# Kernel tuning notes

Hardware: AMD Instinct MI355X
Metric: run time of the kernel (lower is better)

The kernel has to match this reference:

```python
import jax, jax.numpy as jnp
import numpy as np

NEG = 0.01  # leaky_relu negative slope used throughout AttentiveFP


def _seg_softmax(logits, seg, num):
    # softmax over entries grouped by segment id (PyG softmax w/ 1e-16 eps)
    m = jax.ops.segment_max(logits, seg, num_segments=num)
    m = jnp.where(jnp.isfinite(m), m, 0.0)
    e = jnp.exp(logits - m[seg])
    s = jax.ops.segment_sum(e, seg, num_segments=num)
    return e / (s[seg] + 1e-16)


def _gru(x, h, wi, wh, bi, bh):
    # torch.nn.GRUCell math
    gi = x @ wi.T + bi
    gh = h @ wh.T + bh
    ir, iz, inn = jnp.split(gi, 3, axis=-1)
    hr, hz, hn = jnp.split(gh, 3, axis=-1)
    r = jax.nn.sigmoid(ir + hr)
    z = jax.nn.sigmoid(iz + hz)
    n = jnp.tanh(inn + r * hn)
    return (1.0 - z) * n + z * h


def _forward(x, edge_attr, mol_feats, lin1_w, lin1_b, gate_lin1_w, gate_lin2_w, gate_att_l, gate_att_r, gate_bias, grus_wi, grus_wh, grus_bi, grus_bh, atom_w, atom_att_src, atom_att_dst, atom_bias, mol_w, mol_att_src, mol_att_dst, mol_bias, lin2_w, lin2_b, fcm0_w, fcm0_b, fcm1_w, fcm1_b, fcm2_w, fcm2_b, fc0_w, fc0_b, fc1_w, fc1_b, fc2_w, fc2_b, fc3_w, fc3_b, fc4_w, fc4_b, edge_index, batch):
    N = x.shape[0]
    G = mol_feats.shape[0]
    src, dst = edge_index[0], edge_index[1]
    lrelu = lambda v: jax.nn.leaky_relu(v, NEG)
    # AttentiveFP (eval mode: dropout off)
    xh = lrelu(x @ lin1_w.T + lin1_b)  # [N,H]
    # --- GATEConv: edge-conditioned attention, add aggregation ---
    m = lrelu(jnp.concatenate([xh[src], edge_attr], axis=-1) @ gate_lin1_w.T)  # [E,H]
    a = lrelu(m @ gate_att_l + (xh @ gate_att_r)[dst])
    a = _seg_softmax(a, dst, N)
    h = jax.ops.segment_sum((m @ gate_lin2_w.T) * a[:, None], dst, num_segments=N) + gate_bias
    xh = jax.nn.relu(_gru(jax.nn.elu(h), xh, grus_wi[0], grus_wh[0], grus_bi[0], grus_bh[0]))
    # --- GATConv layers (num_layers-1 = 2, heads=1, no self loops) ---
    for l in range(2):
        xl = xh @ atom_w[l].T
        a = lrelu((xl @ atom_att_src[l])[src] + (xl @ atom_att_dst[l])[dst])
        a = _seg_softmax(a, dst, N)
        h = jax.ops.segment_sum(xl[src] * a[:, None], dst, num_segments=N) + atom_bias[l]
        xh = jax.nn.relu(_gru(jax.nn.elu(h), xh, grus_wi[1 + l], grus_wh[1 + l], grus_bi[1 + l], grus_bh[1 + l]))
    # --- attentive graph readout (num_timesteps = 3) ---
    out = jax.nn.relu(jax.ops.segment_sum(xh, batch, num_segments=G))  # [G,H]
    xm = xh @ mol_w.T            # atom-side lin (x fixed across timesteps)
    a_src = xm @ mol_att_src
    for _ in range(3):
        a = lrelu(a_src + ((out @ mol_w.T) @ mol_att_dst)[batch])
        a = _seg_softmax(a, batch, G)
        h = jax.ops.segment_sum(xm * a[:, None], batch, num_segments=G) + mol_bias
        out = jax.nn.relu(_gru(jax.nn.elu(h), out, grus_wi[3], grus_wh[3], grus_bi[3], grus_bh[3]))
    hg = out @ lin2_w.T + lin2_b  # [G,256]
    # --- mol-feature MLP branch (SiLU) ---
    hm = jax.nn.silu(mol_feats @ fcm0_w.T + fcm0_b)
    hm = jax.nn.silu(hm @ fcm1_w.T + fcm1_b)
    hm = jax.nn.silu(hm @ fcm2_w.T + fcm2_b)
    # --- fusion MLP ---
    hg = jnp.concatenate([hg, hm], axis=1)  # [G,512]
    hg = jax.nn.silu(hg @ fc0_w.T + fc0_b)
    hg = jax.nn.silu(hg @ fc1_w.T + fc1_b)
    hg = jax.nn.silu(hg @ fc2_w.T + fc2_b)
    hg = jax.nn.silu(hg @ fc3_w.T + fc3_b)
    return hg @ fc4_w.T + fc4_b  # [G,1]


def setup_inputs() -> dict:
    key = jax.random.key(0)
    ks = iter(jax.random.split(key, 64))
    def W(*shape):
        return jax.random.normal(next(ks), shape, jnp.float32) / np.float32(np.sqrt(shape[-1]))
    def B(*shape):
        return 0.02 * jax.random.normal(next(ks), shape, jnp.float32)
    N, E, G = 131072, 262144, 8192
    Fn, Fe, Fm, H = 64, 16, 200, 256
    return dict(
        x=jax.random.normal(next(ks), (N, Fn), jnp.float32),
        edge_attr=jax.random.normal(next(ks), (E, Fe), jnp.float32),
        mol_feats=jax.random.normal(next(ks), (G, Fm), jnp.float32),
        lin1_w=W(H, Fn), lin1_b=B(H),
        gate_lin1_w=W(H, H + Fe), gate_lin2_w=W(H, H),
        gate_att_l=W(H), gate_att_r=W(H), gate_bias=B(H),
        grus_wi=W(4, 3 * H, H), grus_wh=W(4, 3 * H, H), grus_bi=B(4, 3 * H), grus_bh=B(4, 3 * H),
        atom_w=W(2, H, H), atom_att_src=W(2, H), atom_att_dst=W(2, H), atom_bias=B(2, H),
        mol_w=W(H, H), mol_att_src=W(H), mol_att_dst=W(H), mol_bias=B(H),
        lin2_w=W(H, H), lin2_b=B(H),
        fcm0_w=W(H, Fm), fcm0_b=B(H), fcm1_w=W(H, H), fcm1_b=B(H), fcm2_w=W(H, H), fcm2_b=B(H),
        fc0_w=W(512, 512), fc0_b=B(512), fc1_w=W(512, 512), fc1_b=B(512),
        fc2_w=W(512, 512), fc2_b=B(512), fc3_w=W(128, 512), fc3_b=B(128),
        fc4_w=W(1, 128), fc4_b=B(1),
        edge_index=jax.random.randint(next(ks), (2, E), 0, N),
        batch=jnp.sort(jax.random.randint(next(ks), (N,), 0, G)),
    )


def reference(x, edge_attr, mol_feats, lin1_w, lin1_b, gate_lin1_w, gate_lin2_w, gate_att_l, gate_att_r, gate_bias, grus_wi, grus_wh, grus_bi, grus_bh, atom_w, atom_att_src, atom_att_dst, atom_bias, mol_w, mol_att_src, mol_att_dst, mol_bias, lin2_w, lin2_b, fcm0_w, fcm0_b, fcm1_w, fcm1_b, fcm2_w, fcm2_b, fc0_w, fc0_b, fc1_w, fc1_b, fc2_w, fc2_b, fc3_w, fc3_b, fc4_w, fc4_b, edge_index, batch):
    return _forward(x, edge_attr, mol_feats, lin1_w, lin1_b, gate_lin1_w, gate_lin2_w, gate_att_l, gate_att_r, gate_bias, grus_wi, grus_wh, grus_bi, grus_bh, atom_w, atom_att_src, atom_att_dst, atom_bias, mol_w, mol_att_src, mol_att_dst, mol_bias, lin2_w, lin2_b, fcm0_w, fcm0_b, fcm1_w, fcm1_b, fcm2_w, fcm2_b, fc0_w, fc0_b, fc1_w, fc1_b, fc2_w, fc2_b, fc3_w, fc3_b, fc4_w, fc4_b, edge_index, batch)
```

## Files before the change

kernel.cpp:

```cpp
#include <hip/hip_runtime.h>
#include <hip/hip_bf16.h>
#include <math.h>


typedef unsigned short u16;
typedef u16 u16x8 __attribute__((ext_vector_type(8)));
typedef short s16x8 __attribute__((ext_vector_type(8)));
typedef float f32x4 __attribute__((ext_vector_type(4)));

__device__ __forceinline__ float u2f(u16 u) { return __uint_as_float(((unsigned)u) << 16); }
__device__ __forceinline__ u16 f2u(float f) {
    return __builtin_bit_cast(u16, __float2bfloat16(f));
}

#define NEGS 0.01f

typedef const __attribute__((address_space(1))) unsigned gas1_t;
typedef __attribute__((address_space(3))) unsigned las3_t;
__device__ __forceinline__ void gload16(const void* g, void* l) {
    __builtin_amdgcn_global_load_lds((gas1_t*)g, (las3_t*)l, 16, 0, 0);
}

__device__ __forceinline__ unsigned fkey(float f) {
    unsigned u = __float_as_uint(f);
    return (u & 0x80000000u) ? ~u : (u | 0x80000000u);
}
__device__ __forceinline__ float funkey(unsigned k) {
    return (k & 0x80000000u) ? __uint_as_float(k ^ 0x80000000u) : __uint_as_float(~k);
}
#define KEY_NEG_INF 0x007FFFFFu

static inline int cdiv(int a, int b) { return (a + b - 1) / b; }

__global__ void fill_f32(float* p, float v, size_t n) {
    size_t i = (size_t)blockIdx.x * 256 + threadIdx.x;
    if (i < n) p[i] = v;
}
__global__ void fill_u32(unsigned* p, unsigned v, int n) {
    int i = blockIdx.x * 256 + threadIdx.x;
    if (i < n) p[i] = v;
}
__global__ void fill_km(unsigned* key, float* sum, int n) {
    int i = blockIdx.x * 256 + threadIdx.x;
    if (i < n) { key[i] = KEY_NEG_INF; sum[i] = 0.f; }
}
__global__ void copy_f2b(const float* s, u16* d, size_t n) {
    size_t i = (size_t)blockIdx.x * 256 + threadIdx.x;
    if (i < n) d[i] = f2u(s[i]);
}
__global__ void matvecT_k(const float* W, const float* a, float* v, int K, int Jout) {
    int j = blockIdx.x * 256 + threadIdx.x;
    if (j >= Jout) return;
    float s = 0.f;
    for (int k = 0; k < K; k++) s += W[(size_t)k * Jout + j] * a[k];
    v[j] = s;
}
__global__ void edge_add_lrelu_max(float* elog, const float* r, const int* dsti,
                                   unsigned* key, int E) {
    int i = blockIdx.x * 256 + threadIdx.x;
    if (i < E) {
        int d = dsti[i];
        float v = elog[i] + r[d];
        v = v > 0.f ? v : NEGS * v;
        elog[i] = v;
        atomicMax(&key[d], fkey(v));
    }
}
__global__ void pair_logit_max(float* elog, const float* s, const float* dd,
                               const int* srci, const int* dsti, unsigned* key, int E) {
    int i = blockIdx.x * 256 + threadIdx.x;
    if (i < E) {
        int d = dsti[i];
        float v = s[srci[i]] + dd[d];
        v = v > 0.f ? v : NEGS * v;
        elog[i] = v;
        atomicMax(&key[d], fkey(v));
    }
}
__global__ void node_logit_max(float* nlog, const float* asrc, const float* wg,
                               const int* batch, unsigned* key, int N) {
    int i = blockIdx.x * 256 + threadIdx.x;
    if (i < N) {
        int b = batch[i];
        float v = asrc[i] + wg[b];
        v = v > 0.f ? v : NEGS * v;
        nlog[i] = v;
        atomicMax(&key[b], fkey(v));
    }
}
__global__ void seg_exp_k(const float* logit, const int* idx, const unsigned* key,
                          float* ex, float* sum, int n) {
    int i = blockIdx.x * 256 + threadIdx.x;
    if (i < n) {
        float e = expf(logit[i] - funkey(key[idx[i]]));
        ex[i] = e;
        atomicAdd(&sum[idx[i]], e);
    }
}
__global__ void rowdot2_b(const u16* X, const float* v1, const float* v2,
                          float* o1, float* o2, int M) {
    int r = blockIdx.x * 4 + (threadIdx.x >> 6);
    int lane = threadIdx.x & 63;
    if (r >= M) return;
    const u16* row = X + (size_t)r * 256 + lane * 4;
    float p1 = 0.f, p2 = 0.f;
#pragma unroll
    for (int q = 0; q < 4; q++) {
        float xv = u2f(row[q]);
        p1 += xv * v1[lane * 4 + q];
        if (v2) p2 += xv * v2[lane * 4 + q];
    }
    for (int off = 32; off; off >>= 1) {
        p1 += __shfl_down(p1, off);
        if (v2) p2 += __shfl_down(p2, off);
    }
    if (lane == 0) {
        o1[r] = p1;
        if (v2) o2[r] = p2;
    }
}
__global__ void rowdot_f(const float* X, const float* v1, float* o1, int M) {
    int r = blockIdx.x * 4 + (threadIdx.x >> 6);
    int lane = threadIdx.x & 63;
    if (r >= M) return;
    float4 a = ((const float4*)(X + (size_t)r * 256))[lane];
    float4 b = ((const float4*)v1)[lane];
    float p1 = a.x * b.x + a.y * b.y + a.z * b.z + a.w * b.w;
    for (int off = 32; off; off >>= 1) p1 += __shfl_down(p1, off);
    if (lane == 0) o1[r] = p1;
}
__global__ void fc4_k(const float* X, const float* w, const float* b, float* out, int G) {
    int g = blockIdx.x * 4 + (threadIdx.x >> 6);
    int lane = threadIdx.x & 63;
    if (g >= G) return;
    float2 xv = ((const float2*)(X + (size_t)g * 128))[lane];
    float2 wv = ((const float2*)w)[lane];
    float p = xv.x * wv.x + xv.y * wv.y;
    for (int off = 32; off; off >>= 1) p += __shfl_down(p, off);
    if (lane == 0) out[g] = p + b[0];
}

__global__ void count_dst(const int* dst, int* cnt, int E) {
    int i = blockIdx.x * 256 + threadIdx.x;
    if (i < E) atomicAdd(&cnt[dst[i]], 1);
}
__global__ void scan1(const int* cnt, int* part, int N) {
    __shared__ int sm[256];
    int i = blockIdx.x * 256 + threadIdx.x;
    sm[threadIdx.x] = i < N ? cnt[i] : 0;
    __syncthreads();
    for (int off = 128; off; off >>= 1) {
        if (threadIdx.x < off) sm[threadIdx.x] += sm[threadIdx.x + off];
        __syncthreads();
    }
    if (threadIdx.x == 0) part[blockIdx.x] = sm[0];
}
__global__ void scan2(int* part, int nb) {
    __shared__ int a[1024], b[1024];
    int t = threadIdx.x;
    if (nb > 1024) {
        if (t == 0) {
            int acc = 0;
            for (int i = 0; i < nb; i++) { int v = part[i]; part[i] = acc; acc += v; }
        }
        return;
    }
    int v = t < nb ? part[t] : 0;
    a[t] = v;
    __syncthreads();
    int* cur = a; int* nxt = b;
    for (int off = 1; off < 1024; off <<= 1) {
        int s = cur[t] + (t >= off ? cur[t - off] : 0);
        nxt[t] = s;
        __syncthreads();
        int* tmp = cur; cur = nxt; nxt = tmp;
    }
    if (t < nb) part[t] = cur[t] - v;
}
__global__ void scan3(const int* cnt, const int* part, int* rowstart, int N) {
    __shared__ int a[256], b[256];
    int t = threadIdx.x;
    int i = blockIdx.x * 256 + t;
    int v = i < N ? cnt[i] : 0;
    a[t] = v;
    __syncthreads();
    int* cur = a; int* nxt = b;
    for (int off = 1; off < 256; off <<= 1) {
        int s = cur[t] + (t >= off ? cur[t - off] : 0);
        nxt[t] = s;
        __syncthreads();
        int* tmp = cur; cur = nxt; nxt = tmp;
    }
    if (i < N) rowstart[i] = part[blockIdx.x] + cur[t] - v;
}
__global__ void fill_csr(const int* dst, const int* rowstart, int* fillc,
                         int* eorder, int* erank, int E) {
    int e = blockIdx.x * 256 + threadIdx.x;
    if (e >= E) return;
    int d = dst[e];
    int s = rowstart[d] + atomicAdd(&fillc[d], 1);
    eorder[s] = e;
    erank[e] = s;
}
__global__ void chunk_dlo_k(const int* rowstart, const int* cnt, int N, int Crows,
                            int nch, int* dlo) {
    int c = blockIdx.x * 64 + threadIdx.x;
    if (c >= nch) return;
    int s0 = c * Crows;
    int lo = 0, hi = N;
    while (lo < hi) {
        int mid = (lo + hi) >> 1;
        if (rowstart[mid] + cnt[mid] > s0) hi = mid; else lo = mid + 1;
    }
    dlo[c] = lo;
}
template <int MODE>
__global__ void csr_red(const int* rowstart, const int* cnt, const int* eorder,
                        const float* ex, const float* sum, const int* srcE,
                        const u16* X, const u16* X2, int msplit,
                        int s0, int s1, const int* dlo,
                        u16* outH, u16* outL, int N) {
    int d;
    if (MODE == 1) {
        d = dlo[0] + blockIdx.x;
        if (d >= N) return;
        if (rowstart[d] >= s1) return;
    } else {
        d = blockIdx.x;
        if (d >= N) return;
    }
    int rs = rowstart[d], k = cnt[d];
    int lo = rs, hi = rs + k;
    if (MODE == 1) {
        if (lo < s0) lo = s0;
        if (hi > s1) hi = s1;
        if (lo >= hi) return;
    }
    float den = sum[d] + 1e-16f;
    int c = threadIdx.x;
    float acc = 0.f;
    for (int s = lo; s < hi; s++) {
        int e = eorder[s];
        float av = ex[e] / den;
        const u16* row;
        if (MODE == 0) row = X + (size_t)srcE[e] * 256;
        else if (MODE == 1) row = X + (size_t)(s - s0) * 256;
        else row = (e < msplit) ? X + (size_t)e * 256 : X2 + (size_t)(e - msplit) * 256;
        acc += av * u2f(row[c]);
    }
    size_t o = (size_t)d * 256 + c;
    if (MODE == 1) acc += u2f(outH[o]) + u2f(outL[o]);
    u16 hh = f2u(acc);
    outH[o] = hh;
    outL[o] = f2u(acc - u2f(hh));
}
__global__ void graph_bounds(const int* batch, int* gs, int* ge, int N) {
    int i = blockIdx.x * 256 + threadIdx.x;
    if (i >= N) return;
    int b = batch[i];
    atomicMin(&gs[b], i);
    atomicMax(&ge[b], i + 1);
}
template <bool RELU>
__global__ void seg_red(const int* gs, const int* ge, const u16* X, const float* sc,
                        const float* sum, float* out, int G) {
    int g = blockIdx.x;
    if (g >= G) return;
    int c = threadIdx.x;
    int s = gs[g], e = ge[g];
    float den = sc ? (sum[g] + 1e-16f) : 1.f;
    float acc = 0.f;
    if (s < e)
        for (int i = s; i < e; i++) {
            float v = u2f(X[(size_t)i * 256 + c]);
            if (sc) v *= sc[i] / den;
            acc += v;
        }
    out[(size_t)g * 256 + c] = RELU ? fmaxf(acc, 0.f) : acc;
}

__global__ void pack_w(const float* s1, const float* s2, int K1, int Ksrc,
                       int Nout, int Kp, u16* dst) {
    int idx = blockIdx.x * 256 + threadIdx.x;
    int kiters = Kp >> 5;
    int total = (Nout >> 7) * kiters * 512;
    if (idx >= total) return;
    int c = idx & 511;
    int rest = idx >> 9;
    int ki = rest % kiters, nb = rest / kiters;
    int n = (nb << 7) + (((c >> 6) & 7) << 4) + (c & 15);
    int k0 = (ki << 5) + (((c >> 4) & 3) << 3);
    u16x8 vh, vl;
#pragma unroll
    for (int j = 0; j < 8; j++) {
        int k = k0 + j;
        float f = 0.f;
        if (k < K1) f = s1[(size_t)n * K1 + k];
        else if (k < Ksrc) f = s2[(size_t)n * (Ksrc - K1) + (k - K1)];
        u16 h = f2u(f);
        vh[j] = h;
        vl[j] = f2u(f - u2f(h));
    }
    ((u16x8*)dst)[idx] = vh;
    ((u16x8*)dst)[idx + total] = vl;
}
__global__ void pack_gru_w(const float* wi, const float* wh, u16* dst) {
    int idx = blockIdx.x * 256 + threadIdx.x;
    const int total = 8 * 16 * 512;
    if (idx >= total) return;
    int c = idx & 511, rest = idx >> 9;
    int ki = rest & 15, nb = rest >> 4;
    int n = (nb << 7) + (((c >> 6) & 7) << 4) + (c & 15);
    int k0 = (ki << 5) + (((c >> 4) & 3) << 3);
    int grp = n >> 6, sub = (n >> 4) & 3, ch = grp * 16 + (n & 15);
    u16x8 vh, vl;
#pragma unroll
    for (int j = 0; j < 8; j++) {
        int k = k0 + j;
        float f;
        if (sub < 3) {
            int srow = sub * 256 + ch;
            f = (k < 256) ? wi[(size_t)srow * 256 + k]
                          : wh[(size_t)srow * 256 + (k - 256)];
        } else {
            f = (k < 256) ? 0.f : wh[(size_t)(512 + ch) * 256 + (k - 256)];
        }
        u16 h = f2u(f);
        vh[j] = h;
        vl[j] = f2u(f - u2f(h));
    }
    ((u16x8*)dst)[idx] = vh;
    ((u16x8*)dst)[idx + total] = vl;
}
__global__ void pack_gru_b(const float* bi, const float* bh, float* bp) {
    int n = blockIdx.x * 256 + threadIdx.x;
    if (n >= 1024) return;
    int grp = n >> 6, sub = (n >> 4) & 3, ch = grp * 16 + (n & 15);
    float v;
    if (sub == 0) v = bi[ch] + bh[ch];
    else if (sub == 1) v = bi[256 + ch] + bh[256 + ch];
    else if (sub == 2) v = bi[512 + ch] + bh[512 + ch];
    else v = bh[512 + ch];
    bp[n] = v;
}

struct p8 { u16x8 hi, lo; };
__device__ __forceinline__ u16x8 zero8() {
    u16x8 z;
#pragma unroll
    for (int j = 0; j < 8; j++) z[j] = 0;
    return z;
}
__device__ __forceinline__ p8 sp_zero() { p8 r; r.hi = zero8(); r.lo = zero8(); return r; }
__device__ __forceinline__ p8 sp_b(const u16* p) {
    p8 r;
    r.hi = *(const u16x8*)p;
    r.lo = zero8();
    return r;
}
__device__ __forceinline__ p8 sp_f(const float* p) {
    p8 r;
#pragma unroll
    for (int j = 0; j < 8; j++) {
        float x = p[j];
        u16 h = f2u(x);
        r.hi[j] = h;
        r.lo[j] = f2u(x - u2f(h));
    }
    return r;
}
__device__ __forceinline__ p8 sp_eluf(const float* p) {
    p8 r;
#pragma unroll
    for (int j = 0; j < 8; j++) {
        float x = p[j];
        float e = x > 0.f ? x : expm1f(x);
        u16 h = f2u(e);
        r.hi[j] = h;
        r.lo[j] = f2u(e - u2f(h));
    }
    return r;
}
template <int ALD>
__device__ __forceinline__ p8 ldA(bool valid, int k, int Ksrc, const u16* ab,
                                  const float* af, const float* x2) {
    if (!valid) return sp_zero();
    if (ALD == 1) {
        if (k >= Ksrc) return sp_zero();
        return sp_f(af + k);
    }
    if (ALD == 2 || ALD == 7) {
        if (k < 256) return sp_b(ab + k);
        if (k < 272) return sp_f(x2 + (k - 256));
        return sp_zero();
    }
    if (k < 256) return sp_eluf(af + k);
    return sp_f(x2 + (k - 256));
}
template <int ALD>
__device__ __forceinline__ bool lo_zero(int ki) {
    if (ALD == 2 || ALD == 7) return ki < 8;
    return false;
}
template <int ACT>
__device__ __forceinline__ float actf(float v) {
    if (ACT == 1) return v > 0.f ? v : NEGS * v;
    if (ACT == 3) return v / (1.f + expf(-v));
    return v;
}

template <int ALD, int ACT, int EPI>
__global__ __launch_bounds__(256, 4) void mgemm(
    int M, int Kp, int Ksrc,
    const float* Af, int lda, const u16* Ab, const u16* Ab2,
    const int* gidx, const float* X2f, const u16* Wp, const float* b1,
    float* Cf, u16* Cb, u16* Cb2, int csplit, int ldc,
    const float* attv, float* dotout, const int* didx) {
    __shared__ u16x8 lsAll[2048];
    u16x8* lsAh = lsAll;
    u16x8* lsAl = lsAll + 512;
    u16x8* lsWh = lsAll + 1024;
    u16x8* lsWl = lsAll + 1536;
    const int t = threadIdx.x;
    const int m0 = blockIdx.x * 128;
    const int nb = blockIdx.y;
    const int kiters = Kp >> 5;
    const int r0 = ((t >> 6) << 4) | (t & 15);
    const int kq = ((t >> 4) & 3) << 3;
    const int mA[2] = {m0 + r0, m0 + r0 + 64};
    const u16* abh[2]; const u16* abl[2];
    const float* afr[2]; const float* x2r[2];
    bool val[2];
#pragma unroll
    for (int h = 0; h < 2; h++) {
        int m = mA[h];
        val[h] = (m < M);
        int ms = val[h] ? m : 0;
        abh[h] = nullptr; abl[h] = nullptr; afr[h] = nullptr; x2r[h] = nullptr;
        if constexpr (ALD == 1) {
            afr[h] = Af + (size_t)ms * lda;
        } else if constexpr (ALD == 2) {
            abh[h] = Ab + (size_t)gidx[ms] * 256;
            x2r[h] = X2f + (size_t)ms * 16;
        } else if constexpr (ALD == 7) {
            int e = gidx[ms];
            abh[h] = Ab + (size_t)didx[e] * 256;
            x2r[h] = X2f + (size_t)e * 16;
        } else {
            abh[h] = Ab + (size_t)ms * 256;
            abl[h] = Ab2 + (size_t)ms * 256;
        }
    }
    const int wave = t >> 6, lane = t & 63;
    const int wm = (wave >> 1) << 6, wn = (wave & 1) << 6;
    f32x4 acc[4][4];
#pragma unroll
    for (int i = 0; i < 4; i++)
#pragma unroll
        for (int j = 0; j < 4; j++) {
            acc[i][j][0] = 0.f; acc[i][j][1] = 0.f; acc[i][j][2] = 0.f; acc[i][j][3] = 0.f;
        }
    const u16x8* wh0 = (const u16x8*)Wp + ((size_t)nb * kiters << 9);
    const u16x8* wl0 = wh0 + ((size_t)gridDim.y * kiters << 9);
    for (int ki = 0; ki < kiters; ki++) {
        int kb = (ki << 5) + kq;
        if constexpr (ALD == 6) {
            gload16(abh[0] + kb, &lsAh[t]);
            gload16(abh[1] + kb, &lsAh[t + 256]);
            gload16(abl[0] + kb, &lsAl[t]);
            gload16(abl[1] + kb, &lsAl[t + 256]);
        } else {
            p8 a0 = ldA<ALD>(val[0], kb, Ksrc, abh[0], afr[0], x2r[0]);
            p8 a1 = ldA<ALD>(val[1], kb, Ksrc, abh[1], afr[1], x2r[1]);
            lsAh[t] = a0.hi; lsAl[t] = a0.lo;
            lsAh[t + 256] = a1.hi; lsAl[t + 256] = a1.lo;
        }
        const u16x8* wsh = wh0 + ((size_t)ki << 9);
        const u16x8* wsl = wl0 + ((size_t)ki << 9);
        gload16(wsh + t, &lsWh[t]);
        gload16(wsh + t + 256, &lsWh[t + 256]);
        gload16(wsl + t, &lsWl[t]);
        gload16(wsl + t + 256, &lsWl[t + 256]);
        __syncthreads();
        s16x8 ah[4], al[4], wh[4], wl[4];
#pragma unroll
        for (int f = 0; f < 4; f++) {
            int ai = ((wm >> 4) + f) * 64 + lane;
            int wi = ((wn >> 4) + f) * 64 + lane;
            ah[f] = __builtin_bit_cast(s16x8, lsAh[ai]);
            al[f] = __builtin_bit_cast(s16x8, lsAl[ai]);
            wh[f] = __builtin_bit_cast(s16x8, lsWh[wi]);
            wl[f] = __builtin_bit_cast(s16x8, lsWl[wi]);
        }
        bool skip_lh = lo_zero<ALD>(ki);
#pragma unroll
        for (int fi = 0; fi < 4; fi++)
#pragma unroll
            for (int fj = 0; fj < 4; fj++) {
                acc[fi][fj] = __builtin_amdgcn_mfma_f32_16x16x32_bf16(
                    ah[fi], wh[fj], acc[fi][fj], 0, 0, 0);
                if (!skip_lh)
                    acc[fi][fj] = __builtin_amdgcn_mfma_f32_16x16x32_bf16(
                        al[fi], wh[fj], acc[fi][fj], 0, 0, 0);
                acc[fi][fj] = __builtin_amdgcn_mfma_f32_16x16x32_bf16(
                    ah[fi], wl[fj], acc[fi][fj], 0, 0, 0);
            }
        __syncthreads();
    }
    const int col = lane & 15, quad = lane >> 4;
    const int n_base = nb * 128 + wn;
    u16* lt = (u16*)lsAll;
    const int rowsM = M - m0;
    if constexpr (EPI == 2) {
        float dp[4][4] = {};
#pragma unroll
        for (int fi = 0; fi < 4; fi++)
#pragma unroll
            for (int fj = 0; fj < 4; fj++) {
                int nn = n_base + fj * 16 + col;
                float av = attv[nn];
#pragma unroll
                for (int r = 0; r < 4; r++) {
                    float v = actf<ACT>(acc[fi][fj][r]);
                    dp[fi][r] += v * av;
                    if (Cb) {
                        int lr = wm + fi * 16 + quad * 4 + r;
                        int lc = wn + fj * 16 + col;
                        lt[lr * 128 + lc] = f2u(v);
                    }
                }
            }
#pragma unroll
        for (int fi = 0; fi < 4; fi++)
#pragma unroll
            for (int r = 0; r < 4; r++) {
                float p = dp[fi][r];
                p += __shfl_down(p, 8);
                p += __shfl_down(p, 4);
                p += __shfl_down(p, 2);
                p += __shfl_down(p, 1);
                int mm = m0 + wm + fi * 16 + quad * 4 + r;
                if (col == 0 && mm < M) atomicAdd(dotout + mm, p);
            }
        if (Cb) {
            __syncthreads();
#pragma unroll
            for (int it = 0; it < 8; it++) {
                int idx = it * 256 + t;
                int row = idx >> 4, c8 = idx & 15;
                if (row < rowsM) {
                    int mm = m0 + row;
                    u16* dst = (mm < csplit) ? Cb + (size_t)mm * 256
                                             : Cb2 + (size_t)(mm - csplit) * 256;
                    ((u16x8*)(dst + nb * 128))[c8] = ((u16x8*)lt)[idx];
                }
            }
        }
    } else if constexpr (EPI == 4) {
#pragma unroll
        for (int fj = 0; fj < 4; fj++) {
            int nn = n_base + fj * 16 + col;
            float bb = b1 ? b1[nn] : 0.f;
#pragma unroll
            for (int fi = 0; fi < 4; fi++)
#pragma unroll
                for (int r = 0; r < 4; r++) {
                    float v = acc[fi][fj][r] + bb;
                    float e = v > 0.f ? v : expm1f(v);
                    int lr = wm + fi * 16 + quad * 4 + r;
                    int lc = wn + fj * 16 + col;
                    lt[lr * 128 + lc] = f2u(e);
                }
        }
        __syncthreads();
#pragma unroll
        for (int it = 0; it < 8; it++) {
            int idx = it * 256 + t;
            int row = idx >> 4, c8 = idx & 15;
            if (row < rowsM)
                ((u16x8*)(Cb + (size_t)(m0 + row) * ldc + nb * 128))[c8] =
                    ((u16x8*)lt)[idx];
        }
        __syncthreads();
#pragma unroll
        for (int fj = 0; fj < 4; fj++) {
            int nn = n_base + fj * 16 + col;
            float bb = b1 ? b1[nn] : 0.f;
#pragma unroll
            for (int fi = 0; fi < 4; fi++)
#pragma unroll
                for (int r = 0; r < 4; r++) {
                    float v = acc[fi][fj][r] + bb;
                    float e = v > 0.f ? v : expm1f(v);
                    u16 hh = f2u(e);
                    int lr = wm + fi * 16 + quad * 4 + r;
                    int lc = wn + fj * 16 + col;
                    lt[lr * 128 + lc] = f2u(e - u2f(hh));
                }
        }
        __syncthreads();
#pragma unroll
        for (int it = 0; it < 8; it++) {
            int idx = it * 256 + t;
            int row = idx >> 4, c8 = idx & 15;
            if (row < rowsM)
                ((u16x8*)(Cb2 + (size_t)(m0 + row) * ldc + nb * 128))[c8] =
                    ((u16x8*)lt)[idx];
        }
    } else if constexpr (EPI == 1) {
#pragma unroll
        for (int fj = 0; fj < 4; fj++) {
            int nn = n_base + fj * 16 + col;
            float bb = b1 ? b1[nn] : 0.f;
#pragma unroll
            for (int fi = 0; fi < 4; fi++)
#pragma unroll
                for (int r = 0; r < 4; r++) {
                    float v = actf<ACT>(acc[fi][fj][r] + bb);
                    int lr = wm + fi * 16 + quad * 4 + r;
                    int lc = wn + fj * 16 + col;
                    lt[lr * 128 + lc] = f2u(v);
                }
        }
        __syncthreads();
#pragma unroll
        for (int it = 0; it < 8; it++) {
            int idx = it * 256 + t;
            int row = idx >> 4, c8 = idx & 15;
            if (row < rowsM)
                ((u16x8*)(Cb + (size_t)(m0 + row) * ldc + nb * 128))[c8] =
                    ((u16x8*)lt)[idx];
        }
    } else {
#pragma unroll
        for (int fj = 0; fj < 4; fj++) {
            int nn = n_base + fj * 16 + col;
            float bb = b1 ? b1[nn] : 0.f;
#pragma unroll
            for (int fi = 0; fi < 4; fi++)
#pragma unroll
                for (int r = 0; r < 4; r++) {
                    int mm = m0 + wm + fi * 16 + quad * 4 + r;
                    if (mm >= M) continue;
                    float v = actf<ACT>(acc[fi][fj][r] + bb);
                    Cf[(size_t)mm * ldc + nn] = v;
                }
        }
    }
}

template <int ALD, bool HB, bool OB>
__global__ __launch_bounds__(256, 4) void mgemm_gru(
    int M, const float* Af, const u16* Ab, const u16* Ab2, const float* X2f,
    const u16* Wp, const float* bp, const u16* hb, const float* hf,
    float* of, u16* ob) {
    __shared__ u16x8 lsAll[2048];
    u16x8* lsAh = lsAll;
    u16x8* lsAl = lsAll + 512;
    u16x8* lsWh = lsAll + 1024;
    u16x8* lsWl = lsAll + 1536;
    const int t = threadIdx.x;
    const int m0 = blockIdx.x * 128;
    const int nb = blockIdx.y;
    const int r0 = ((t >> 6) << 4) | (t & 15);
    const int kq = ((t >> 4) & 3) << 3;
    const int mA[2] = {m0 + r0, m0 + r0 + 64};
    const u16* ehr[2]; const u16* elr[2]; const u16* xhr[2];
    const float* afr[2]; const float* x2r[2];
    bool val[2];
#pragma unroll
    for (int h = 0; h < 2; h++) {
        int m = mA[h];
        val[h] = (m < M);
        int ms = val[h] ? m : 0;
        ehr[h] = nullptr; elr[h] = nullptr; xhr[h] = nullptr;
        afr[h] = nullptr; x2r[h] = nullptr;
        if constexpr (ALD == 5) {
            ehr[h] = Ab + (size_t)ms * 256;
            elr[h] = Ab2 + (size_t)ms * 256;
            xhr[h] = hb + (size_t)ms * 256;
        } else {
            afr[h] = Af + (size_t)ms * 256;
            x2r[h] = X2f + (size_t)ms * 256;
        }
    }
    const int wave = t >> 6, lane = t & 63;
    const int wm = (wave >> 1) << 6, wn = (wave & 1) << 6;
    f32x4 acc[4][4];
#pragma unroll
    for (int i = 0; i < 4; i++)
#pragma unroll
        for (int j = 0; j < 4; j++) {
            acc[i][j][0] = 0.f; acc[i][j][1] = 0.f; acc[i][j][2] = 0.f; acc[i][j][3] = 0.f;
        }
    const u16x8* wh0 = (const u16x8*)Wp + ((size_t)nb * 16 << 9);
    const u16x8* wl0 = (const u16x8*)Wp + (size_t)(8 * 16 * 512) + ((size_t)nb * 16 << 9);
    for (int ki = 0; ki < 16; ki++) {
        int kb = (ki << 5) + kq;
        if constexpr (ALD == 5) {
            const u16* p0 = kb < 256 ? ehr[0] + kb : xhr[0] + (kb - 256);
            const u16* p1 = kb < 256 ? ehr[1] + kb : xhr[1] + (kb - 256);
            gload16(p0, &lsAh[t]);
            gload16(p1, &lsAh[t + 256]);
            if (ki < 8) {
                gload16(elr[0] + kb, &lsAl[t]);
                gload16(elr[1] + kb, &lsAl[t + 256]);
            }
        } else {
            p8 a0 = ldA<4>(val[0], kb, 512, nullptr, afr[0], x2r[0]);
            p8 a1 = ldA<4>(val[1], kb, 512, nullptr, afr[1], x2r[1]);
            lsAh[t] = a0.hi; lsAl[t] = a0.lo;
            lsAh[t + 256] = a1.hi; lsAl[t + 256] = a1.lo;
        }
        const u16x8* wsh = wh0 + ((size_t)ki << 9);
        const u16x8* wsl = wl0 + ((size_t)ki << 9);
        gload16(wsh + t, &lsWh[t]);
        gload16(wsh + t + 256, &lsWh[t + 256]);
        gload16(wsl + t, &lsWl[t]);
        gload16(wsl + t + 256, &lsWl[t + 256]);
        __syncthreads();
        s16x8 ah[4], al[4], wh[4], wl[4];
#pragma unroll
        for (int f = 0; f < 4; f++) {
            int ai = ((wm >> 4) + f) * 64 + lane;
            int wi = ((wn >> 4) + f) * 64 + lane;
            ah[f] = __builtin_bit_cast(s16x8, lsAh[ai]);
            al[f] = __builtin_bit_cast(s16x8, lsAl[ai]);
            wh[f] = __builtin_bit_cast(s16x8, lsWh[wi]);
            wl[f] = __builtin_bit_cast(s16x8, lsWl[wi]);
        }
        bool skip_lh = (ALD == 5) ? (ki >= 8) : false;
        bool hn_zero = (ki < 8);
#pragma unroll
        for (int fi = 0; fi < 4; fi++)
#pragma unroll
            for (int fj = 0; fj < 4; fj++) {
                if (fj == 3 && hn_zero) continue;
                acc[fi][fj] = __builtin_amdgcn_mfma_f32_16x16x32_bf16(
                    ah[fi], wh[fj], acc[fi][fj], 0, 0, 0);
                if (!skip_lh)
                    acc[fi][fj] = __builtin_amdgcn_mfma_f32_16x16x32_bf16(
                        al[fi], wh[fj], acc[fi][fj], 0, 0, 0);
                acc[fi][fj] = __builtin_amdgcn_mfma_f32_16x16x32_bf16(
                    ah[fi], wl[fj], acc[fi][fj], 0, 0, 0);
            }
        __syncthreads();
    }
    const int col = lane & 15, quad = lane >> 4;
    const int nbase = nb * 128 + wn;
    float br = bp[nbase + col];
    float bz = bp[nbase + 16 + col];
    float bn = bp[nbase + 32 + col];
    float bhn = bp[nbase + 48 + col];
    int ch = (nb * 2 + (wn >> 6)) * 16 + col;
    int lc = ((wn >> 6) << 4) + col;
    u16* lt = (u16*)lsAll;
    float* ft = (float*)lsAll;
#pragma unroll
    for (int fi = 0; fi < 4; fi++)
#pragma unroll
        for (int r = 0; r < 4; r++) {
            int m = m0 + wm + fi * 16 + quad * 4 + r;
            if (m >= M) continue;
            float rs = acc[fi][0][r] + br;
            float zs = acc[fi][1][r] + bz;
            float nsv = acc[fi][2][r] + bn;
            float hnv = acc[fi][3][r] + bhn;
            float rr = 1.f / (1.f + expf(-rs));
            float zz = 1.f / (1.f + expf(-zs));
            float nn = tanhf(nsv - hnv + rr * hnv);
            float ho = HB ? u2f(hb[(size_t)m * 256 + ch]) : hf[(size_t)m * 256 + ch];
            float o = fmaxf((1.f - zz) * nn + zz * ho, 0.f);
            int lr = wm + fi * 16 + quad * 4 + r;
            if (OB) lt[lr * 32 + lc] = f2u(o);
            else ft[lr * 32 + lc] = o;
        }
    __syncthreads();
    const int rowsM = M - m0;
    if (OB) {
#pragma unroll
        for (int it = 0; it < 2; it++) {
            int idx = it * 256 + t;
            int row = idx >> 2, c8 = idx & 3;
            if (row < rowsM)
                ((u16x8*)(ob + (size_t)(m0 + row) * 256 + nb * 32))[c8] =
                    ((u16x8*)lt)[idx];
        }
    } else {
#pragma unroll
        for (int it = 0; it < 4; it++) {
            int idx = it * 256 + t;
            int row = idx >> 3, c4 = idx & 7;
            if (row < rowsM)
                ((float4*)(of + (size_t)(m0 + row) * 256 + nb * 32))[c4] =
                    ((float4*)ft)[idx];
        }
    }
}

extern "C" void kernel_launch(void* const* d_in, const int* in_sizes, int n_in,
                              void* d_out, int out_size, void* d_ws, size_t ws_size,
                              hipStream_t stream) {
    const float* x = (const float*)d_in[0];
    const float* edge_attr = (const float*)d_in[1];
    const float* mol_feats = (const float*)d_in[2];
    const float* lin1_w = (const float*)d_in[3];
    const float* lin1_b = (const float*)d_in[4];
    const float* gate_lin1_w = (const float*)d_in[5];
    const float* gate_lin2_w = (const float*)d_in[6];
    const float* gate_att_l = (const float*)d_in[7];
    const float* gate_att_r = (const float*)d_in[8];
    const float* gate_bias = (const float*)d_in[9];
    const float* grus_wi = (const float*)d_in[10];
    const float* grus_wh = (const float*)d_in[11];
    const float* grus_bi = (const float*)d_in[12];
    const float* grus_bh = (const float*)d_in[13];
    const float* atom_w = (const float*)d_in[14];
    const float* atom_att_src = (const float*)d_in[15];
    const float* atom_att_dst = (const float*)d_in[16];
    const float* atom_bias = (const float*)d_in[17];
    const float* mol_w = (const float*)d_in[18];
    const float* mol_att_src = (const float*)d_in[19];
    const float* mol_att_dst = (const float*)d_in[20];
    const float* mol_bias = (const float*)d_in[21];
    const float* lin2_w = (const float*)d_in[22];
    const float* lin2_b = (const float*)d_in[23];
    const float* fcm0_w = (const float*)d_in[24];
    const float* fcm0_b = (const float*)d_in[25];
    const float* fcm1_w = (const float*)d_in[26];
    const float* fcm1_b = (const float*)d_in[27];
    const float* fcm2_w = (const float*)d_in[28];
    const float* fcm2_b = (const float*)d_in[29];
    const float* fc0_w = (const float*)d_in[30];
    const float* fc0_b = (const float*)d_in[31];
    const float* fc1_w = (const float*)d_in[32];
    const float* fc1_b = (const float*)d_in[33];
    const float* fc2_w = (const float*)d_in[34];
    const float* fc2_b = (const float*)d_in[35];
    const float* fc3_w = (const float*)d_in[36];
    const float* fc3_b = (const float*)d_in[37];
    const float* fc4_w = (const float*)d_in[38];
    const float* fc4_b = (const float*)d_in[39];
    const int* edge_index = (const int*)d_in[40];
    const int* batch = (const int*)d_in[41];
    float* out_final = (float*)d_out;

    const int N = in_sizes[0] / 64;
    const int E = in_sizes[1] / 16;
    const int G = in_sizes[2] / 200;
    const int* srcE = edge_index;
    const int* dstE = edge_index + E;

    char* base = (char*)d_ws;
    size_t off = 0;
    auto alloc = [&](size_t bytes) -> char* {
        char* p = base + off;
        off += (bytes + 255) & ~(size_t)255;
        return p;
    };
    u16* xhA = (u16*)alloc((size_t)N * 512);
    u16* haggH = (u16*)alloc((size_t)N * 512);
    u16* haggL = (u16*)alloc((size_t)N * 512);
    float* outg = (float*)alloc((size_t)G * 1024);
    float* hgrb = (float*)alloc((size_t)G * 1024);
    float* elog = (float*)alloc((size_t)E * 4);
    float* eexp = (float*)alloc((size_t)E * 4);
    unsigned* nkey = (unsigned*)alloc((size_t)N * 4);
    float* nsum = (float*)alloc((size_t)N * 4);
    float* ns1 = (float*)alloc((size_t)N * 4);
    float* ns2 = (float*)alloc((size_t)N * 4);
    unsigned* gkey = (unsigned*)alloc((size_t)G * 4);
    float* gsum = (float*)alloc((size_t)G * 4);
    float* wgb = (float*)alloc((size_t)G * 4);
    float* vbuf = (float*)alloc(4096);
    int* ecnt = (int*)alloc((size_t)N * 4);
    int* efill = (int*)alloc((size_t)N * 4);
    int* erowst = (int*)alloc((size_t)N * 4);
    int* eorder = (int*)alloc((size_t)E * 4);
    int* erank = (int*)alloc((size_t)E * 4);
    int* spart = (int*)alloc(4096 * 4);
    int* cdlo = (int*)alloc(((size_t)E / 128 + 2) * 4);
    int* gs = (int*)alloc((size_t)G * 4);
    int* ge = (int*)alloc((size_t)G * 4);
    u16* pk_lin1 = (u16*)alloc(256 * 64 * 2 * 2);
    u16* pk_g1 = (u16*)alloc(256 * 288 * 2 * 2);
    u16* pk_g2 = (u16*)alloc(256 * 256 * 2 * 2);
    u16* pk_gruF[4];
    float* bp_gru[4];
    for (int l = 0; l < 4; l++) {
        pk_gruF[l] = (u16*)alloc(1024 * 512 * 2 * 2);
        bp_gru[l] = (float*)alloc(1024 * 4);
    }
    u16* pk_atom[2];
    for (int l = 0; l < 2; l++) pk_atom[l] = (u16*)alloc(256 * 256 * 2 * 2);
    u16* pk_mol = (u16*)alloc(256 * 256 * 2 * 2);
    u16* pk_lin2 = (u16*)alloc(256 * 256 * 2 * 2);
    u16* pk_fcm0 = (u16*)alloc(256 * 224 * 2 * 2);
    u16* pk_fcm1 = (u16*)alloc(256 * 256 * 2 * 2);
    u16* pk_fcm2 = (u16*)alloc(256 * 256 * 2 * 2);
    u16* pk_fc0 = (u16*)alloc(512 * 512 * 2 * 2);
    u16* pk_fc1 = (u16*)alloc(512 * 512 * 2 * 2);
    u16* pk_fc2 = (u16*)alloc(512 * 512 * 2 * 2);
    u16* pk_fc3 = (u16*)alloc(128 * 512 * 2 * 2);
    size_t fixed_core = off;
    if (fixed_core + (size_t)2 * 1024 * 1024 > ws_size) {
        fill_f32<<<cdiv(out_size, 256), 256, 0, stream>>>(out_final, (float)ws_size,
                                                          (size_t)out_size);
        return;
    }
    u16* xhB = nullptr;
    bool use_pp = false;
    if (ws_size - off >= (size_t)N * 512 + (size_t)2 * 1024 * 1024) {
        xhB = (u16*)alloc((size_t)N * 512);
        use_pp = true;
    }
    size_t workbytes = ws_size - off;
    char* workp = base + off;
    int Mc = (int)((workbytes / (use_pp ? 1024 : 2048)) & ~(size_t)127);
    if (Mc > N) Mc = N;
    if (Mc < 128) Mc = 128;
    u16* ehi = (u16*)workp;
    u16* elo = ehi + (size_t)Mc * 256;
    float* htmp = (float*)(workp + (size_t)Mc * 1024);
    float* cbuf = (float*)workp;
    u16* mt1 = nullptr; u16* mt2 = nullptr; int msplit = 0x7fffffff;
    if (workbytes >= (size_t)E * 512) { mt1 = (u16*)workp; msplit = E; }
    else if (use_pp) {
        if (N >= E) { mt1 = xhB; msplit = E; }
        else if ((size_t)N * 512 + workbytes >= (size_t)E * 512) {
            mt1 = xhB; msplit = N; mt2 = (u16*)workp;
        }
    }
    bool gate_store = (mt1 != nullptr);
    size_t crows_sz = workbytes / 512;
    if (crows_sz > (size_t)E) crows_sz = (size_t)E;
    int Crows = (int)(crows_sz & ~(size_t)127);
    if (Crows < 128) Crows = 128;
    int nch = cdiv(E, Crows);
    u16* mchunk = (u16*)workp;
    float* fbufA = (float*)haggH;
    float* fbufB = fbufA + (size_t)G * 512;
    float* fbufC = fbufB + (size_t)G * 512;
    float* f128 = fbufC + (size_t)G * 512;
    float* hm1 = f128 + (size_t)G * 128;
    float* hm2 = hm1 + (size_t)G * 256;

    auto pack = [&](const float* s1, const float* s2, int K1, int Ksrc, int Nout,
                    int Kp, u16* dst) {
        int total = (Nout >> 7) * (Kp >> 5) * 512;
        pack_w<<<cdiv(total, 256), 256, 0, stream>>>(s1, s2, K1, Ksrc, Nout, Kp, dst);
    };
    pack(lin1_w, nullptr, 64, 64, 256, 64, pk_lin1);
    pack(gate_lin1_w, nullptr, 272, 272, 256, 288, pk_g1);
    pack(gate_lin2_w, nullptr, 256, 256, 256, 256, pk_g2);
    for (int l = 0; l < 4; l++) {
        pack_gru_w<<<cdiv(8 * 16 * 512, 256), 256, 0, stream>>>(
            grus_wi + (size_t)l * 768 * 256, grus_wh + (size_t)l * 768 * 256,
            pk_gruF[l]);
        pack_gru_b<<<4, 256, 0, stream>>>(grus_bi + (size_t)l * 768,
                                          grus_bh + (size_t)l * 768, bp_gru[l]);
    }
    for (int l = 0; l < 2; l++)
        pack(atom_w + (size_t)l * 256 * 256, nullptr, 256, 256, 256, 256, pk_atom[l]);
    pack(mol_w, nullptr, 256, 256, 256, 256, pk_mol);
    pack(lin2_w, nullptr, 256, 256, 256, 256, pk_lin2);
    pack(fcm0_w, nullptr, 200, 200, 256, 224, pk_fcm0);
    pack(fcm1_w, nullptr, 256, 256, 256, 256, pk_fcm1);
    pack(fcm2_w, nullptr, 256, 256, 256, 256, pk_fcm2);
    pack(fc0_w, nullptr, 512, 512, 512, 512, pk_fc0);
    pack(fc1_w, nullptr, 512, 512, 512, 512, pk_fc1);
    pack(fc2_w, nullptr, 512, 512, 512, 512, pk_fc2);
    pack(fc3_w, nullptr, 512, 512, 128, 512, pk_fc3);

    int nbk = cdiv(N, 256);
    fill_u32<<<nbk, 256, 0, stream>>>((unsigned*)ecnt, 0u, N);
    fill_u32<<<nbk, 256, 0, stream>>>((unsigned*)efill, 0u, N);
    count_dst<<<cdiv(E, 256), 256, 0, stream>>>(dstE, ecnt, E);
    scan1<<<nbk, 256, 0, stream>>>(ecnt, spart, N);
    scan2<<<1, 1024, 0, stream>>>(spart, nbk);
    scan3<<<nbk, 256, 0, stream>>>(ecnt, spart, erowst, N);
    fill_csr<<<cdiv(E, 256), 256, 0, stream>>>(dstE, erowst, efill, eorder, erank, E);
    fill_u32<<<cdiv(G, 256), 256, 0, stream>>>((unsigned*)gs, (unsigned)N, G);
    fill_u32<<<cdiv(G, 256), 256, 0, stream>>>((unsigned*)ge, 0u, G);
    graph_bounds<<<nbk, 256, 0, stream>>>(batch, gs, ge, N);

    u16* xh_cur = xhA;
    u16* xh_nxt = xhB;

    auto node_gru = [&](int l, const u16* Wpre, const float* bpre) {
        for (int c0 = 0; c0 < N; c0 += Mc) {
            int Ms = N - c0 < Mc ? N - c0 : Mc;
            int gx = cdiv(Ms, 128);
            mgemm<6, 0, 4><<<dim3(gx, 2), 256, 0, stream>>>(Ms, 256, 256,
                nullptr, 0, haggH + (size_t)c0 * 256, haggL + (size_t)c0 * 256,
                nullptr, nullptr, Wpre, bpre,
                nullptr, ehi, elo, 0, 256, nullptr, nullptr, nullptr);
            if (use_pp) {
                mgemm_gru<5, true, true><<<dim3(gx, 8), 256, 0, stream>>>(Ms,
                    nullptr, ehi, elo, nullptr, pk_gruF[l], bp_gru[l],
                    xh_cur + (size_t)c0 * 256, nullptr,
                    nullptr, xh_nxt + (size_t)c0 * 256);
            } else {
                mgemm_gru<5, true, false><<<dim3(gx, 8), 256, 0, stream>>>(Ms,
                    nullptr, ehi, elo, nullptr, pk_gruF[l], bp_gru[l],
                    xh_cur + (size_t)c0 * 256, nullptr,
                    htmp, nullptr);
                copy_f2b<<<(int)(((size_t)Ms * 256 + 255) / 256), 256, 0, stream>>>(
                    htmp, xh_cur + (size_t)c0 * 256, (size_t)Ms * 256);
            }
        }
        if (use_pp) { u16* t2 = xh_cur; xh_cur = xh_nxt; xh_nxt = t2; }
    };

    mgemm<1, 1, 1><<<dim3(cdiv(N, 128), 2), 256, 0, stream>>>(N, 64, 64,
        x, 64, nullptr, nullptr, nullptr, nullptr, pk_lin1, lin1_b,
        nullptr, xh_cur, nullptr, 0, 256, nullptr, nullptr, nullptr);

    fill_f32<<<cdiv(E, 256), 256, 0, stream>>>(elog, 0.f, (size_t)E);
    mgemm<2, 1, 2><<<dim3(cdiv(E, 128), 2), 256, 0, stream>>>(E, 288, 272,
        nullptr, 0, xh_cur, nullptr, srcE, edge_attr, pk_g1, nullptr,
        nullptr, gate_store ? mt1 : nullptr, mt2, msplit, 256,
        gate_att_l, elog, nullptr);
    rowdot2_b<<<cdiv(N, 4), 256, 0, stream>>>(xh_cur, gate_att_r, nullptr, ns1, nullptr, N);
    fill_km<<<nbk, 256, 0, stream>>>(nkey, nsum, N);
    edge_add_lrelu_max<<<cdiv(E, 256), 256, 0, stream>>>(elog, ns1, dstE, nkey, E);
    seg_exp_k<<<cdiv(E, 256), 256, 0, stream>>>(elog, dstE, nkey, eexp, nsum, E);
    if (gate_store) {
        csr_red<2><<<N, 256, 0, stream>>>(erowst, ecnt, eorder, eexp, nsum, nullptr,
            mt1, mt2, msplit, 0, E, nullptr, haggH, haggL, N);
    } else {
        fill_u32<<<cdiv(N * 256, 256), 256, 0, stream>>>((unsigned*)haggH, 0u, N * 256);
        chunk_dlo_k<<<cdiv(nch, 64), 64, 0, stream>>>(erowst, ecnt, N, Crows, nch, cdlo);
        for (int c = 0; c < nch; c++) {
            int s0 = c * Crows;
            int s1 = s0 + Crows < E ? s0 + Crows : E;
            int Ms = s1 - s0;
            mgemm<7, 1, 1><<<dim3(cdiv(Ms, 128), 2), 256, 0, stream>>>(Ms, 288, 272,
                nullptr, 0, xh_cur, nullptr, eorder + s0, edge_attr, pk_g1, nullptr,
                nullptr, mchunk, nullptr, 0x7fffffff, 256,
                nullptr, nullptr, srcE);
            csr_red<1><<<Crows, 256, 0, stream>>>(erowst, ecnt, eorder, eexp, nsum,
                nullptr, mchunk, nullptr, 0, s0, s1, cdlo + c, haggH, haggL, N);
        }
    }
    node_gru(0, pk_g2, gate_bias);

    for (int l = 0; l < 2; l++) {
        const float* aw = atom_w + (size_t)l * 256 * 256;
        matvecT_k<<<1, 256, 0, stream>>>(aw, atom_att_src + (size_t)l * 256, vbuf, 256, 256);
        matvecT_k<<<1, 256, 0, stream>>>(aw, atom_att_dst + (size_t)l * 256, vbuf + 256, 256, 256);
        rowdot2_b<<<cdiv(N, 4), 256, 0, stream>>>(xh_cur, vbuf, vbuf + 256, ns1, ns2, N);
        fill_km<<<nbk, 256, 0, stream>>>(nkey, nsum, N);
        pair_logit_max<<<cdiv(E, 256), 256, 0, stream>>>(elog, ns1, ns2, srcE, dstE, nkey, E);
        seg_exp_k<<<cdiv(E, 256), 256, 0, stream>>>(elog, dstE, nkey, eexp, nsum, E);
        csr_red<0><<<N, 256, 0, stream>>>(erowst, ecnt, eorder, eexp, nsum, srcE,
            xh_cur, nullptr, 0, 0, 0, nullptr, haggH, haggL, N);
        node_gru(1 + l, pk_atom[l], atom_bias + (size_t)l * 256);
    }

    seg_red<true><<<G, 256, 0, stream>>>(gs, ge, xh_cur, nullptr, nullptr, outg, G);
    matvecT_k<<<1, 256, 0, stream>>>(mol_w, mol_att_dst, vbuf, 256, 256);
    matvecT_k<<<1, 256, 0, stream>>>(mol_w, mol_att_src, vbuf + 256, 256, 256);
    rowdot2_b<<<cdiv(N, 4), 256, 0, stream>>>(xh_cur, vbuf + 256, nullptr, ns1, nullptr, N);
    float* ogc = outg;
    float* ogn = hgrb;
    int McG = Mc < G ? Mc : G;
    for (int t = 0; t < 3; t++) {
        rowdot_f<<<cdiv(G, 4), 256, 0, stream>>>(ogc, vbuf, wgb, G);
        fill_km<<<cdiv(G, 256), 256, 0, stream>>>(gkey, gsum, G);
        node_logit_max<<<nbk, 256, 0, stream>>>(elog, ns1, wgb, batch, gkey, N);
        seg_exp_k<<<nbk, 256, 0, stream>>>(elog, batch, gkey, eexp, gsum, N);
        seg_red<false><<<G, 256, 0, stream>>>(gs, ge, xh_cur, eexp, gsum, ogn, G);
        for (int c0 = 0; c0 < G; c0 += McG) {
            int Ms = G - c0 < McG ? G - c0 : McG;
            int gx = cdiv(Ms, 128);
            mgemm<1, 0, 0><<<dim3(gx, 2), 256, 0, stream>>>(Ms, 256, 256,
                ogn + (size_t)c0 * 256, 256, nullptr, nullptr, nullptr, nullptr,
                pk_mol, mol_bias, cbuf, nullptr, nullptr, 0, 256,
                nullptr, nullptr, nullptr);
            mgemm_gru<4, false, false><<<dim3(gx, 8), 256, 0, stream>>>(Ms,
                cbuf, nullptr, nullptr, ogc + (size_t)c0 * 256, pk_gruF[3], bp_gru[3],
                nullptr, ogc + (size_t)c0 * 256, ogn + (size_t)c0 * 256, nullptr);
        }
        float* tt = ogc; ogc = ogn; ogn = tt;
    }

    int gG = cdiv(G, 128);
    mgemm<1, 0, 0><<<dim3(gG, 2), 256, 0, stream>>>(G, 256, 256, ogc, 256,
        nullptr, nullptr, nullptr, nullptr, pk_lin2, lin2_b,
        fbufA, nullptr, nullptr, 0, 512, nullptr, nullptr, nullptr);
    mgemm<1, 3, 0><<<dim3(gG, 2), 256, 0, stream>>>(G, 224, 200, mol_feats, 200,
        nullptr, nullptr, nullptr, nullptr, pk_fcm0, fcm0_b,
        hm1, nullptr, nullptr, 0, 256, nullptr, nullptr, nullptr);
    mgemm<1, 3, 0><<<dim3(gG, 2), 256, 0, stream>>>(G, 256, 256, hm1, 256,
        nullptr, nullptr, nullptr, nullptr, pk_fcm1, fcm1_b,
        hm2, nullptr, nullptr, 0, 256, nullptr, nullptr, nullptr);
    mgemm<1, 3, 0><<<dim3(gG, 2), 256, 0, stream>>>(G, 256, 256, hm2, 256,
        nullptr, nullptr, nullptr, nullptr, pk_fcm2, fcm2_b,
        fbufA + 256, nullptr, nullptr, 0, 512, nullptr, nullptr, nullptr);
    mgemm<1, 3, 0><<<dim3(gG, 4), 256, 0, stream>>>(G, 512, 512, fbufA, 512,
        nullptr, nullptr, nullptr, nullptr, pk_fc0, fc0_b,
        fbufB, nullptr, nullptr, 0, 512, nullptr, nullptr, nullptr);
    mgemm<1, 3, 0><<<dim3(gG, 4), 256, 0, stream>>>(G, 512, 512, fbufB, 512,
        nullptr, nullptr, nullptr, nullptr, pk_fc1, fc1_b,
        fbufC, nullptr, nullptr, 0, 512, nullptr, nullptr, nullptr);
    mgemm<1, 3, 0><<<dim3(gG, 4), 256, 0, stream>>>(G, 512, 512, fbufC, 512,
        nullptr, nullptr, nullptr, nullptr, pk_fc2, fc2_b,
        fbufB, nullptr, nullptr, 0, 512, nullptr, nullptr, nullptr);
    mgemm<1, 3, 0><<<dim3(gG, 1), 256, 0, stream>>>(G, 512, 512, fbufB, 512,
        nullptr, nullptr, nullptr, nullptr, pk_fc3, fc3_b,
        f128, nullptr, nullptr, 0, 128, nullptr, nullptr, nullptr);
    fc4_k<<<cdiv(G, 4), 256, 0, stream>>>(f128, fc4_w, fc4_b, out_final, G);
}
```

Before: 5.589 ms.

## Replace dot atomics with per-slot partials, merge matvecs, drop erank

```diff
diff --git a/kernel.cpp b/kernel.cpp
--- a/kernel.cpp
+++ b/kernel.cpp
@@ -55,12 +55,29 @@
     for (int k = 0; k < K; k++) s += W[(size_t)k * Jout + j] * a[k];
     v[j] = s;
 }
-__global__ void edge_add_lrelu_max(float* elog, const float* r, const int* dsti,
-                                   unsigned* key, int E) {
+__global__ void matvecT2_k(const float* W1, const float* a1, float* o1,
+                           const float* W2, const float* a2, float* o2,
+                           int K, int Jout) {
+    int j = blockIdx.x * 256 + threadIdx.x;
+    if (j < Jout) {
+        float s = 0.f;
+        for (int k = 0; k < K; k++) s += W1[(size_t)k * Jout + j] * a1[k];
+        o1[j] = s;
+    } else if (j < 2 * Jout) {
+        int jj = j - Jout;
+        float s = 0.f;
+        for (int k = 0; k < K; k++) s += W2[(size_t)k * Jout + jj] * a2[k];
+        o2[jj] = s;
+    }
+}
+__global__ void edge_add_lrelu_max(const float* dp4, float* elog, const float* r,
+                                   const int* dsti, unsigned* key, int E) {
     int i = blockIdx.x * 256 + threadIdx.x;
     if (i < E) {
         int d = dsti[i];
-        float v = elog[i] + r[d];
+        float p = (dp4[i] + dp4[(size_t)E + i]) +
+                  (dp4[(size_t)2 * E + i] + dp4[(size_t)3 * E + i]);
+        float v = p + r[d];
         v = v > 0.f ? v : NEGS * v;
         elog[i] = v;
         atomicMax(&key[d], fkey(v));
@@ -102,11 +119,12 @@
     int r = blockIdx.x * 4 + (threadIdx.x >> 6);
     int lane = threadIdx.x & 63;
     if (r >= M) return;
-    const u16* row = X + (size_t)r * 256 + lane * 4;
+    ushort4 rv = *(const ushort4*)(X + (size_t)r * 256 + lane * 4);
+    u16 q4[4] = {rv.x, rv.y, rv.z, rv.w};
     float p1 = 0.f, p2 = 0.f;
 #pragma unroll
     for (int q = 0; q < 4; q++) {
-        float xv = u2f(row[q]);
+        float xv = u2f(q4[q]);
         p1 += xv * v1[lane * 4 + q];
         if (v2) p2 += xv * v2[lane * 4 + q];
     }
@@ -194,13 +212,12 @@
     if (i < N) rowstart[i] = part[blockIdx.x] + cur[t] - v;
 }
 __global__ void fill_csr(const int* dst, const int* rowstart, int* fillc,
-                         int* eorder, int* erank, int E) {
+                         int* eorder, int E) {
     int e = blockIdx.x * 256 + threadIdx.x;
     if (e >= E) return;
     int d = dst[e];
     int s = rowstart[d] + atomicAdd(&fillc[d], 1);
     eorder[s] = e;
-    erank[e] = s;
 }
 __global__ void chunk_dlo_k(const int* rowstart, const int* cnt, int N, int Crows,
                             int nch, int* dlo) {
@@ -530,6 +547,7 @@
                     }
                 }
             }
+        const size_t slot = (size_t)(nb * 2 + (wn >> 6)) * (size_t)M;
 #pragma unroll
         for (int fi = 0; fi < 4; fi++)
 #pragma unroll
@@ -540,7 +558,7 @@
                 p += __shfl_down(p, 2);
                 p += __shfl_down(p, 1);
                 int mm = m0 + wm + fi * 16 + quad * 4 + r;
-                if (col == 0 && mm < M) atomicAdd(dotout + mm, p);
+                if (col == 0 && mm < M) dotout[slot + mm] = p;
             }
         if (Cb) {
             __syncthreads();
@@ -865,6 +883,7 @@
     float* hgrb = (float*)alloc((size_t)G * 1024);
     float* elog = (float*)alloc((size_t)E * 4);
     float* eexp = (float*)alloc((size_t)E * 4);
+    float* dotp = (float*)alloc((size_t)E * 16);
     unsigned* nkey = (unsigned*)alloc((size_t)N * 4);
     float* nsum = (float*)alloc((size_t)N * 4);
     float* ns1 = (float*)alloc((size_t)N * 4);
@@ -877,7 +896,6 @@
     int* efill = (int*)alloc((size_t)N * 4);
     int* erowst = (int*)alloc((size_t)N * 4);
     int* eorder = (int*)alloc((size_t)E * 4);
-    int* erank = (int*)alloc((size_t)E * 4);
     int* spart = (int*)alloc(4096 * 4);
     int* cdlo = (int*)alloc(((size_t)E / 128 + 2) * 4);
     int* gs = (int*)alloc((size_t)G * 4);
@@ -979,7 +997,7 @@
     scan1<<<nbk, 256, 0, stream>>>(ecnt, spart, N);
     scan2<<<1, 1024, 0, stream>>>(spart, nbk);
     scan3<<<nbk, 256, 0, stream>>>(ecnt, spart, erowst, N);
-    fill_csr<<<cdiv(E, 256), 256, 0, stream>>>(dstE, erowst, efill, eorder, erank, E);
+    fill_csr<<<cdiv(E, 256), 256, 0, stream>>>(dstE, erowst, efill, eorder, E);
     fill_u32<<<cdiv(G, 256), 256, 0, stream>>>((unsigned*)gs, (unsigned)N, G);
     fill_u32<<<cdiv(G, 256), 256, 0, stream>>>((unsigned*)ge, 0u, G);
     graph_bounds<<<nbk, 256, 0, stream>>>(batch, gs, ge, N);
@@ -1016,14 +1034,13 @@
         x, 64, nullptr, nullptr, nullptr, nullptr, pk_lin1, lin1_b,
         nullptr, xh_cur, nullptr, 0, 256, nullptr, nullptr, nullptr);
 
-    fill_f32<<<cdiv(E, 256), 256, 0, stream>>>(elog, 0.f, (size_t)E);
     mgemm<2, 1, 2><<<dim3(cdiv(E, 128), 2), 256, 0, stream>>>(E, 288, 272,
         nullptr, 0, xh_cur, nullptr, srcE, edge_attr, pk_g1, nullptr,
         nullptr, gate_store ? mt1 : nullptr, mt2, msplit, 256,
-        gate_att_l, elog, nullptr);
+        gate_att_l, dotp, nullptr);
     rowdot2_b<<<cdiv(N, 4), 256, 0, stream>>>(xh_cur, gate_att_r, nullptr, ns1, nullptr, N);
     fill_km<<<nbk, 256, 0, stream>>>(nkey, nsum, N);
-    edge_add_lrelu_max<<<cdiv(E, 256), 256, 0, stream>>>(elog, ns1, dstE, nkey, E);
+    edge_add_lrelu_max<<<cdiv(E, 256), 256, 0, stream>>>(dotp, elog, ns1, dstE, nkey, E);
     seg_exp_k<<<cdiv(E, 256), 256, 0, stream>>>(elog, dstE, nkey, eexp, nsum, E);
     if (gate_store) {
         csr_red<2><<<N, 256, 0, stream>>>(erowst, ecnt, eorder, eexp, nsum, nullptr,
@@ -1047,8 +1064,9 @@
 
     for (int l = 0; l < 2; l++) {
         const float* aw = atom_w + (size_t)l * 256 * 256;
-        matvecT_k<<<1, 256, 0, stream>>>(aw, atom_att_src + (size_t)l * 256, vbuf, 256, 256);
-        matvecT_k<<<1, 256, 0, stream>>>(aw, atom_att_dst + (size_t)l * 256, vbuf + 256, 256, 256);
+        matvecT2_k<<<2, 256, 0, stream>>>(aw, atom_att_src + (size_t)l * 256, vbuf,
+                                          aw, atom_att_dst + (size_t)l * 256, vbuf + 256,
+                                          256, 256);
         rowdot2_b<<<cdiv(N, 4), 256, 0, stream>>>(xh_cur, vbuf, vbuf + 256, ns1, ns2, N);
         fill_km<<<nbk, 256, 0, stream>>>(nkey, nsum, N);
         pair_logit_max<<<cdiv(E, 256), 256, 0, stream>>>(elog, ns1, ns2, srcE, dstE, nkey, E);
@@ -1059,8 +1077,8 @@
     }
 
     seg_red<true><<<G, 256, 0, stream>>>(gs, ge, xh_cur, nullptr, nullptr, outg, G);
-    matvecT_k<<<1, 256, 0, stream>>>(mol_w, mol_att_dst, vbuf, 256, 256);
-    matvecT_k<<<1, 256, 0, stream>>>(mol_w, mol_att_src, vbuf + 256, 256, 256);
+    matvecT2_k<<<2, 256, 0, stream>>>(mol_w, mol_att_dst, vbuf,
+                                      mol_w, mol_att_src, vbuf + 256, 256, 256);
     rowdot2_b<<<cdiv(N, 4), 256, 0, stream>>>(xh_cur, vbuf + 256, nullptr, ns1, nullptr, N);
     float* ogc = outg;
     float* ogn = hgrb;
```

Result: faster. 5.434 ms (-2.8%).
